# Kernel optimization log

Hardware: AMD Instinct MI355X
Metric: run time of the kernel (lower is better)

Reference implementation:

```python
import jax, jax.numpy as jnp
import numpy as np

NUM_EMBEDDINGS = 8192
EMBEDDING_DIM = 256
COMMITMENT_WEIGHT = 0.25
EMA_DECAY = 0.99
EPSILON = 1e-05


def setup_inputs() -> dict:
    key = jax.random.key(0)
    k1, k2 = jax.random.split(key)
    z = jax.random.normal(k1, (8, 4096, EMBEDDING_DIM), dtype=jnp.float32)
    # xavier-uniform-ish codebook init
    limit = np.sqrt(6.0 / (NUM_EMBEDDINGS + EMBEDDING_DIM))
    embeddings = jax.random.uniform(
        k2, (NUM_EMBEDDINGS, EMBEDDING_DIM), dtype=jnp.float32,
        minval=-limit, maxval=limit)
    ema_cluster_size = jnp.zeros((NUM_EMBEDDINGS,), dtype=jnp.float32)
    ema_embed_sum = embeddings.copy()
    return {
        'z': z,
        'embeddings': embeddings,
        'ema_cluster_size': ema_cluster_size,
        'ema_embed_sum': ema_embed_sum,
    }


def reference(z, embeddings, ema_cluster_size, ema_embed_sum):
    input_shape = z.shape
    D = input_shape[-1]
    z_flat = z.reshape(-1, D)                                  # [N, D]

    # Squared euclidean distances via expansion: ||z||^2 + ||e||^2 - 2 z.e
    z_sq = jnp.sum(z_flat * z_flat, axis=1, keepdims=True)     # [N, 1]
    e_sq = jnp.sum(embeddings * embeddings, axis=1)            # [K]
    ze = jnp.matmul(z_flat, embeddings.T)                      # [N, K]
    distances = z_sq + e_sq - 2.0 * ze                          # [N, K]
    indices = jnp.argmin(distances, axis=1)                    # [N] int

    z_q_flat = embeddings[indices]                             # [N, D] gather
    z_q = z_q_flat.reshape(input_shape)

    # commitment loss = mse(stop_grad(z_q), z)
    diff = jax.lax.stop_gradient(z_q) - z
    commitment_loss = jnp.mean(diff * diff) * COMMITMENT_WEIGHT

    # straight-through estimator
    z_q_st = z + jax.lax.stop_gradient(z_q - z)

    # EMA codebook update (functional version of the in-place buffer update)
    ones = jnp.ones_like(indices, dtype=embeddings.dtype)
    cluster_size = jax.ops.segment_sum(ones, indices, num_segments=NUM_EMBEDDINGS)
    embed_sum = jax.ops.segment_sum(z_flat, indices, num_segments=NUM_EMBEDDINGS)
    new_ema_cluster_size = EMA_DECAY * ema_cluster_size + (1.0 - EMA_DECAY) * cluster_size
    new_ema_embed_sum = EMA_DECAY * ema_embed_sum + (1.0 - EMA_DECAY) * embed_sum
    new_embeddings = new_ema_embed_sum / (new_ema_cluster_size[:, None] + EPSILON)

    indices_out = indices.reshape(input_shape[:-1])
    return (z_q_st, indices_out, commitment_loss,
            new_embeddings, new_ema_cluster_size, new_ema_embed_sum)
```

## Files before the change

### kernel.cpp

```cpp
#include <hip/hip_runtime.h>
#include <hip/hip_bf16.h>
#include <math.h>

#define N_TOK   32768
#define DIM     256
#define KC      8192

#define OUT_ZQ    0
#define OUT_IDX   8388608
#define OUT_LOSS  8421376
#define OUT_NEMB  8421377
#define OUT_CS    10518529
#define OUT_SUM   10526721

#define MARGIN  8e-3f
#define FLAGCAP 16384

typedef __attribute__((ext_vector_type(8))) __bf16 bf16x8;
typedef __attribute__((ext_vector_type(4))) float f32x4;

__device__ __forceinline__ void gload16(const void* g, void* l) {
  __builtin_amdgcn_global_load_lds((const __attribute__((address_space(1))) void*)g,
                                   (__attribute__((address_space(3))) void*)l, 16, 0, 0);
}

__device__ __forceinline__ float np_sumsq256(const float* __restrict__ p, int lane) {
  const int l = lane & 15;
  const int h = l >> 3;
  const int j = l & 7;
  const float* a = p + h * 128 + j;
  float x = a[0];
  float r = __fmul_rn(x, x);
  #pragma unroll
  for (int i = 1; i < 16; ++i) {
    x = a[8 * i];
    r = __fadd_rn(r, __fmul_rn(x, x));
  }
  r = __fadd_rn(r, __shfl_down(r, 1));
  r = __fadd_rn(r, __shfl_down(r, 2));
  r = __fadd_rn(r, __shfl_down(r, 4));
  float hi = __shfl(r, (lane & 48) | 8);
  return __fadd_rn(r, hi);
}

__global__ void vq_prep(const float* __restrict__ emb, float* __restrict__ esq,
                        short* __restrict__ esp2) {
  const int t = threadIdx.x;
  const int code = blockIdx.x * 8 + (t >> 5);
  const int p = t & 31, j = p >> 2, g = p & 3;
  const float* src = emb + (size_t)code * DIM + j * 32 + g * 8;
  const float4 v0 = *(const float4*)src;
  const float4 v1 = *(const float4*)(src + 4);
  const float xf[8] = {v0.x, v0.y, v0.z, v0.w, v1.x, v1.y, v1.z, v1.w};
  bf16x8 hb;
  #pragma unroll
  for (int e = 0; e < 8; ++e) hb[e] = (__bf16)xf[e];
  const int c = code & 15, sub = (code >> 4) & 3, ct = code >> 6;
  const int slot = (g + (c >> 1)) & 3;
  char* dst = (char*)esp2 + (size_t)ct * 32768 + ((sub * 8 + j) << 10) + c * 64 + slot * 16;
  *(bf16x8*)dst = hb;
  if (t < 128) {
    const int code2 = blockIdx.x * 8 + (t >> 4);
    const float s = np_sumsq256(emb + (size_t)code2 * DIM, t & 63);
    if ((t & 15) == 0) esq[code2] = s;
  }
}

__global__ void vq_transpose(const float* __restrict__ emb, float* __restrict__ embT) {
  __shared__ float t[64][65];
  const int tid = threadIdx.x;
  const int bc  = blockIdx.x & 127;
  const int bk  = blockIdx.x >> 7;
  const int cc0 = bc << 6, kc0 = bk << 6;
  const int col = tid & 63, qr = tid >> 6;
  #pragma unroll
  for (int i = 0; i < 16; ++i) {
    const int row = i * 4 + qr;
    t[row][col] = emb[(size_t)(cc0 + row) * DIM + kc0 + col];
  }
  __syncthreads();
  #pragma unroll
  for (int i = 0; i < 16; ++i) {
    const int krow = i * 4 + qr;
    embT[(size_t)(kc0 + krow) * KC + cc0 + col] = t[col][krow];
  }
}

__global__ void vq_init(int* __restrict__ hist, int* __restrict__ cnt) {
  const int i = blockIdx.x * blockDim.x + threadIdx.x;
  hist[i] = 0;
  if (i == 0) cnt[0] = 0;
}

__launch_bounds__(256, 4)
__global__ void vq_mfma(const float* __restrict__ z,
                        const short* __restrict__ esp,
                        const float* __restrict__ esq,
                        float* __restrict__ pb1,
                        int* __restrict__ pi1,
                        float* __restrict__ pb2) {
  __shared__ __align__(16) char lds[32768];
  const int tid  = threadIdx.x;
  const int lane = tid & 63;
  const int w    = tid >> 6;
  const int l15  = lane & 15;
  const int g    = lane >> 4;
  const int rt   = blockIdx.x >> 1;
  const int kh   = blockIdx.x & 1;
  const int rowbase = rt * 128 + w * 32;
  const int u0 = kh * 128, u1 = u0 + 128;
  const int gx = (g + (l15 >> 1)) & 3;
  const char* espb = (const char*)esp;

#define STAGE(U, BUFB)                                                           \
  {                                                                              \
    _Pragma("unroll")                                                            \
    for (int q_ = 0; q_ < 4; ++q_) {                                             \
      const int so_ = (((w << 2) + q_) << 10);                                   \
      gload16(espb + (size_t)(U) * 16384 + so_ + (lane << 4),                    \
              (void*)(lds + (BUFB) + so_));                                      \
    }                                                                            \
  }

  STAGE(u0, 0);

  bf16x8 Ahi[2][8];
  #pragma unroll
  for (int s = 0; s < 2; ++s) {
    const float* zr = z + (size_t)(rowbase + s * 16 + l15) * DIM + g * 8;
    #pragma unroll
    for (int c = 0; c < 8; ++c) {
      const float4 v0 = *(const float4*)(zr + c * 32);
      const float4 v1 = *(const float4*)(zr + c * 32 + 4);
      const float xf[8] = {v0.x, v0.y, v0.z, v0.w, v1.x, v1.y, v1.z, v1.w};
      #pragma unroll
      for (int e = 0; e < 8; ++e) Ahi[s][c][e] = (__bf16)xf[e];
    }
  }

  __syncthreads();

  float b1[2][4], b2[2][4];
  int   i1[2][4];
  #pragma unroll
  for (int s = 0; s < 2; ++s)
    #pragma unroll
    for (int r = 0; r < 4; ++r) { b1[s][r] = 3.4e38f; b2[s][r] = 3.4e38f; i1[s][r] = 0x7fffffff; }

  int bp = 0;
  for (int u = u0; u < u1; ++u) {
    if (u + 1 < u1) STAGE(u + 1, (bp ^ 1) << 14);

    const float eq0 = esq[(u << 5) + l15];
    const float eq1 = esq[(u << 5) + 16 + l15];

    f32x4 acc00 = (f32x4){0.f, 0.f, 0.f, 0.f};
    f32x4 acc01 = (f32x4){0.f, 0.f, 0.f, 0.f};
    f32x4 acc10 = (f32x4){0.f, 0.f, 0.f, 0.f};
    f32x4 acc11 = (f32x4){0.f, 0.f, 0.f, 0.f};

    {
      const char* base = lds + (bp << 14);
      #pragma unroll
      for (int j_ = 0; j_ < 8; ++j_) {
        const char* bq_ = base + (j_ << 10) + (l15 << 6) + (gx << 4);
        const bf16x8 bF0 = *(const bf16x8*)(bq_);
        const bf16x8 bF1 = *(const bf16x8*)(bq_ + 8192);
        acc00 = __builtin_amdgcn_mfma_f32_16x16x32_bf16(Ahi[0][j_], bF0, acc00, 0, 0, 0);
        acc01 = __builtin_amdgcn_mfma_f32_16x16x32_bf16(Ahi[0][j_], bF1, acc01, 0, 0, 0);
        acc10 = __builtin_amdgcn_mfma_f32_16x16x32_bf16(Ahi[1][j_], bF0, acc10, 0, 0, 0);
        acc11 = __builtin_amdgcn_mfma_f32_16x16x32_bf16(Ahi[1][j_], bF1, acc11, 0, 0, 0);
      }
    }

    const int code0 = (u << 5) + l15;
    const int code1 = code0 + 16;
    #pragma unroll
    for (int r = 0; r < 4; ++r) {
      const float sc = fmaf(-2.f, acc00[r], eq0);
      const bool lt = sc < b1[0][r];
      b2[0][r] = fminf(b2[0][r], fmaxf(sc, b1[0][r]));
      i1[0][r] = lt ? code0 : i1[0][r];
      b1[0][r] = fminf(b1[0][r], sc);
    }
    #pragma unroll
    for (int r = 0; r < 4; ++r) {
      const float sc = fmaf(-2.f, acc01[r], eq1);
      const bool lt = sc < b1[0][r];
      b2[0][r] = fminf(b2[0][r], fmaxf(sc, b1[0][r]));
      i1[0][r] = lt ? code1 : i1[0][r];
      b1[0][r] = fminf(b1[0][r], sc);
    }
    #pragma unroll
    for (int r = 0; r < 4; ++r) {
      const float sc = fmaf(-2.f, acc10[r], eq0);
      const bool lt = sc < b1[1][r];
      b2[1][r] = fminf(b2[1][r], fmaxf(sc, b1[1][r]));
      i1[1][r] = lt ? code0 : i1[1][r];
      b1[1][r] = fminf(b1[1][r], sc);
    }
    #pragma unroll
    for (int r = 0; r < 4; ++r) {
      const float sc = fmaf(-2.f, acc11[r], eq1);
      const bool lt = sc < b1[1][r];
      b2[1][r] = fminf(b2[1][r], fmaxf(sc, b1[1][r]));
      i1[1][r] = lt ? code1 : i1[1][r];
      b1[1][r] = fminf(b1[1][r], sc);
    }
    __syncthreads();
    bp ^= 1;
  }

  #pragma unroll
  for (int s = 0; s < 2; ++s) {
    #pragma unroll
    for (int r = 0; r < 4; ++r) {
      float v1 = b1[s][r], v2 = b2[s][r];
      int   j1 = i1[s][r];
      #pragma unroll
      for (int off = 1; off < 16; off <<= 1) {
        const float o1 = __shfl_xor(v1, off);
        const int   oj = __shfl_xor(j1, off);
        const float o2 = __shfl_xor(v2, off);
        v2 = fminf(fminf(v2, o2), fmaxf(v1, o1));
        const bool tk = (o1 < v1) || (o1 == v1 && oj < j1);
        j1 = tk ? oj : j1;
        v1 = fminf(v1, o1);
      }
      if (l15 == 0) {
        const int rr = kh * N_TOK + rowbase + s * 16 + (g << 2) + r;
        pb1[rr] = v1; pi1[rr] = j1; pb2[rr] = v2;
      }
    }
  }
}

__global__ void vq_merge(const float* __restrict__ pb1, const int* __restrict__ pi1,
                         const float* __restrict__ pb2, int* __restrict__ idxf,
                         int* __restrict__ flag, int* __restrict__ cnt) {
  const int gi = blockIdx.x * blockDim.x + threadIdx.x;
  const float va = pb1[gi],        vb = pb1[N_TOK + gi];
  const int   ia = pi1[gi],        ib = pi1[N_TOK + gi];
  const float v2a = pb2[gi],       v2b = pb2[N_TOK + gi];
  float v1, v2; int i1;
  if (va < vb || (va == vb && ia < ib)) { v1 = va; i1 = ia; v2 = fminf(v2a, vb); }
  else                                  { v1 = vb; i1 = ib; v2 = fminf(v2b, va); }
  idxf[gi] = i1;
  if (v2 - v1 < MARGIN) {
    const int p = atomicAdd(cnt, 1);
    if (p < FLAGCAP) flag[p] = gi;
  }
}

__global__ void vq_rescan2(const float* __restrict__ z,
                           const float* __restrict__ embT,
                           const float* __restrict__ esq,
                           const int* __restrict__ flag,
                           const int* __restrict__ cnt,
                           float* __restrict__ rpv,
                           int* __restrict__ rpi) {
  __shared__ __align__(16) float zT[DIM][16];
  __shared__ float zsq_sh[16];
  __shared__ float rv[4][16];
  __shared__ int   ri[4][16];
  __shared__ int   rown[16];
  int n = *cnt; if (n > FLAGCAP) n = FLAGCAP;
  const int tid = threadIdx.x;
  const int lane = tid & 63, wv = tid >> 6;
  const int nb = (n + 15) >> 4;
  const int ntask = nb * 8;
  for (int task = blockIdx.x; task < ntask; task += gridDim.x) {
    const int bb = task >> 3, cz = task & 7;
    __syncthreads();
    if (tid < 16) rown[tid] = flag[min(bb * 16 + tid, n - 1)];
    __syncthreads();
    #pragma unroll
    for (int rr = 0; rr < 16; ++rr) zT[tid][rr] = z[(size_t)rown[rr] * DIM + tid];
    {
      const int rr = tid >> 4;
      const float s = np_sumsq256(z + (size_t)rown[rr] * DIM, lane);
      if ((tid & 15) == 0) zsq_sh[rr] = s;
    }
    __syncthreads();

    float a[16][4];
    #pragma unroll
    for (int rr = 0; rr < 16; ++rr)
      #pragma unroll
      for (int q = 0; q < 4; ++q) a[rr][q] = 0.f;

    const int c0 = cz * 1024 + tid;
    #pragma unroll 2
    for (int k = 0; k < DIM; ++k) {
      const float* rk = embT + (size_t)k * KC + c0;
      const float e0 = rk[0], e1 = rk[256], e2 = rk[512], e3 = rk[768];
      const f32x4 z0 = *(const f32x4*)&zT[k][0];
      const f32x4 z1 = *(const f32x4*)&zT[k][4];
      const f32x4 z2 = *(const f32x4*)&zT[k][8];
      const f32x4 z3 = *(const f32x4*)&zT[k][12];
      #pragma unroll
      for (int r4 = 0; r4 < 4; ++r4) {
        a[r4][0] = fmaf(z0[r4], e0, a[r4][0]);
        a[r4][1] = fmaf(z0[r4], e1, a[r4][1]);
        a[r4][2] = fmaf(z0[r4], e2, a[r4][2]);
        a[r4][3] = fmaf(z0[r4], e3, a[r4][3]);
        a[4 + r4][0] = fmaf(z1[r4], e0, a[4 + r4][0]);
        a[4 + r4][1] = fmaf(z1[r4], e1, a[4 + r4][1]);
        a[4 + r4][2] = fmaf(z1[r4], e2, a[4 + r4][2]);
        a[4 + r4][3] = fmaf(z1[r4], e3, a[4 + r4][3]);
        a[8 + r4][0] = fmaf(z2[r4], e0, a[8 + r4][0]);
        a[8 + r4][1] = fmaf(z2[r4], e1, a[8 + r4][1]);
        a[8 + r4][2] = fmaf(z2[r4], e2, a[8 + r4][2]);
        a[8 + r4][3] = fmaf(z2[r4], e3, a[8 + r4][3]);
        a[12 + r4][0] = fmaf(z3[r4], e0, a[12 + r4][0]);
        a[12 + r4][1] = fmaf(z3[r4], e1, a[12 + r4][1]);
        a[12 + r4][2] = fmaf(z3[r4], e2, a[12 + r4][2]);
        a[12 + r4][3] = fmaf(z3[r4], e3, a[12 + r4][3]);
      }
    }

    #pragma unroll
    for (int rr = 0; rr < 16; ++rr) {
      float bv = 3.4e38f; int bi = 0x7fffffff;
      #pragma unroll
      for (int q = 0; q < 4; ++q) {
        const int code = cz * 1024 + q * 256 + tid;
        const float D = __fsub_rn(__fadd_rn(zsq_sh[rr], esq[code]), __fmul_rn(2.f, a[rr][q]));
        if (D < bv) { bv = D; bi = code; }
      }
      #pragma unroll
      for (int off = 32; off; off >>= 1) {
        const float ov = __shfl_down(bv, off);
        const int   oi = __shfl_down(bi, off);
        if (ov < bv || (ov == bv && oi < bi)) { bv = ov; bi = oi; }
      }
      if (lane == 0) { rv[wv][rr] = bv; ri[wv][rr] = bi; }
    }
    __syncthreads();
    if (tid < 16) {
      const int fi = bb * 16 + tid;
      if (fi < n) {
        float fv = rv[0][tid]; int fx = ri[0][tid];
        #pragma unroll
        for (int q = 1; q < 4; ++q)
          if (rv[q][tid] < fv || (rv[q][tid] == fv && ri[q][tid] < fx)) { fv = rv[q][tid]; fx = ri[q][tid]; }
        rpv[fi * 8 + cz] = fv; rpi[fi * 8 + cz] = fx;
      }
    }
  }
}

__global__ void vq_rmerge(const int* __restrict__ flag, const int* __restrict__ cnt,
                          const float* __restrict__ rpv, const int* __restrict__ rpi,
                          int* __restrict__ idxf) {
  int n = *cnt; if (n > FLAGCAP) n = FLAGCAP;
  const int fi = blockIdx.x * blockDim.x + threadIdx.x;
  if (fi >= n) return;
  float bv = rpv[fi * 8]; int bi = rpi[fi * 8];
  #pragma unroll
  for (int c = 1; c < 8; ++c) {
    const float v = rpv[fi * 8 + c]; const int ix = rpi[fi * 8 + c];
    if (v < bv || (v == bv && ix < bi)) { bv = v; bi = ix; }
  }
  idxf[flag[fi]] = bi;
}

__global__ void vq_gather(const float* __restrict__ z, const float* __restrict__ emb,
                          const int* __restrict__ idxf, float* __restrict__ out,
                          float* __restrict__ lossp, int* __restrict__ hist) {
  __shared__ float part[4];
  const int tid = threadIdx.x, lane = tid & 63, w = tid >> 6;
  const int row = blockIdx.x * 4 + w;
  const int code = idxf[row];
  const float4 zv = *(const float4*)(z + (size_t)row * DIM + lane * 4);
  const float4 ev = *(const float4*)(emb + (size_t)code * DIM + lane * 4);
  float4 d, o;
  d.x = ev.x - zv.x; d.y = ev.y - zv.y; d.z = ev.z - zv.z; d.w = ev.w - zv.w;
  o.x = zv.x + d.x;  o.y = zv.y + d.y;  o.z = zv.z + d.z;  o.w = zv.w + d.w;
  *(float4*)(out + OUT_ZQ + (size_t)row * DIM + lane * 4) = o;
  float sq = fmaf(d.x, d.x, fmaf(d.y, d.y, fmaf(d.z, d.z, d.w * d.w)));
  #pragma unroll
  for (int off = 32; off; off >>= 1) sq += __shfl_down(sq, off);
  if (lane == 0) {
    part[w] = sq;
    atomicAdd(hist + code, 1);
    out[OUT_IDX + row] = (float)code;
  }
  __syncthreads();
  if (tid == 0) lossp[blockIdx.x] = (part[0] + part[1]) + (part[2] + part[3]);
}

__global__ void vq_prefix(const float* __restrict__ ema_cs, int* __restrict__ hist,
                          int* __restrict__ base, int* __restrict__ cursor,
                          const float* __restrict__ lossp, float* __restrict__ out) {
  __shared__ int ps[256];
  __shared__ float lp[4];
  const int t = threadIdx.x;

  float ls = 0.f;
  #pragma unroll
  for (int j = 0; j < 8; ++j) {
    const float4 v = *(const float4*)(lossp + t * 32 + j * 4);
    ls += (v.x + v.y) + (v.z + v.w);
  }
  #pragma unroll
  for (int off = 32; off; off >>= 1) ls += __shfl_down(ls, off);
  if ((t & 63) == 0) lp[t >> 6] = ls;

  int loc[32]; int s = 0;
  #pragma unroll
  for (int j = 0; j < 32; ++j) { loc[j] = hist[t * 32 + j]; s += loc[j]; }
  ps[t] = s;
  __syncthreads();
  if (t == 0)
    out[OUT_LOSS] = 0.25f * (((lp[0] + lp[1]) + (lp[2] + lp[3])) * (1.f / 8388608.f));
  for (int off = 1; off < 256; off <<= 1) {
    const int v = (t >= off) ? ps[t - off] : 0;
    __syncthreads();
    ps[t] += v;
    __syncthreads();
  }
  int run = ps[t] - s;
  #pragma unroll
  for (int j = 0; j < 32; ++j) {
    const int i = t * 32 + j;
    base[i] = run; cursor[i] = run;
    out[OUT_CS + i] = 0.99f * ema_cs[i] + 0.01f * (float)loc[j];
    run += loc[j];
  }
}

__global__ void vq_slot(const int* __restrict__ idxf, int* __restrict__ cursor,
                        int* __restrict__ rowlist) {
  const int gi = blockIdx.x * blockDim.x + threadIdx.x;
  const int code = idxf[gi];
  const int p = atomicAdd(cursor + code, 1);
  rowlist[p] = gi;
}

__global__ void vq_embsum(const float* __restrict__ z, const float* __restrict__ ema_sum,
                          const int* __restrict__ rowlist, const int* __restrict__ base,
                          const int* __restrict__ hist, float* __restrict__ out) {
  const int code = blockIdx.x;
  const int lane = threadIdx.x;
  const int b = base[code], n = hist[code];
  float a0 = 0.f, a1 = 0.f, a2 = 0.f, a3 = 0.f;
  for (int i = 0; i < n; ++i) {
    const float4 v = *(const float4*)(z + (size_t)rowlist[b + i] * DIM + lane * 4);
    a0 += v.x; a1 += v.y; a2 += v.z; a3 += v.w;
  }
  const float4 es = *(const float4*)(ema_sum + (size_t)code * DIM + lane * 4);
  const float s0 = 0.99f * es.x + 0.01f * a0;
  const float s1 = 0.99f * es.y + 0.01f * a1;
  const float s2 = 0.99f * es.z + 0.01f * a2;
  const float s3 = 0.99f * es.w + 0.01f * a3;
  float* sp = out + OUT_SUM + (size_t)code * DIM + lane * 4;
  sp[0] = s0; sp[1] = s1; sp[2] = s2; sp[3] = s3;
  const float cs = out[OUT_CS + code] + 1e-5f;
  float* np_ = out + OUT_NEMB + (size_t)code * DIM + lane * 4;
  np_[0] = s0 / cs; np_[1] = s1 / cs; np_[2] = s2 / cs; np_[3] = s3 / cs;
}

extern "C" void kernel_launch(void* const* d_in, const int* in_sizes, int n_in,
                              void* d_out, int out_size, void* d_ws, size_t ws_size,
                              hipStream_t stream) {
  const float* z      = (const float*)d_in[0];
  const float* emb    = (const float*)d_in[1];
  const float* emacs  = (const float*)d_in[2];
  const float* emasum = (const float*)d_in[3];
  float* out = (float*)d_out;
  float* ws  = (float*)d_ws;

  float* esq     = ws;
  int*   idxf    = (int*)(ws + 8192);
  int*   flag    = (int*)(ws + 40960);
  int*   cnt     = (int*)(ws + 57344);
  int*   hist    = (int*)(ws + 57600);
  int*   base    = (int*)(ws + 65792);
  int*   cursor  = (int*)(ws + 73984);
  int*   rowlist = (int*)(ws + 82176);
  float* pb1     = ws + 114944;
  int*   pi1     = (int*)(ws + 180480);
  float* pb2     = ws + 246016;
  short* esp2    = (short*)(ws + 311552);
  float* embT    = ws + 1360128;
  float* rpv     = ws + 3457280;
  int*   rpi     = (int*)(ws + 3588352);
  float* lossp   = pb1;

  vq_prep<<<KC / 8, 256, 0, stream>>>(emb, esq, esp2);
  vq_transpose<<<512, 256, 0, stream>>>(emb, embT);
  vq_init<<<KC / 256, 256, 0, stream>>>(hist, cnt);

  vq_mfma<<<512, 256, 0, stream>>>(z, esp2, esq, pb1, pi1, pb2);
  vq_merge<<<N_TOK / 256, 256, 0, stream>>>(pb1, pi1, pb2, idxf, flag, cnt);
  vq_rescan2<<<1024, 256, 0, stream>>>(z, embT, esq, flag, cnt, rpv, rpi);
  vq_rmerge<<<FLAGCAP / 256, 256, 0, stream>>>(flag, cnt, rpv, rpi, idxf);

  vq_gather<<<N_TOK / 4, 256, 0, stream>>>(z, emb, idxf, out, lossp, hist);
  vq_prefix<<<1, 256, 0, stream>>>(emacs, hist, base, cursor, lossp, out);
  vq_slot<<<N_TOK / 256, 256, 0, stream>>>(idxf, cursor, rowlist);
  vq_embsum<<<KC, 64, 0, stream>>>(z, emasum, rowlist, base, hist, out);
}
```

Baseline: 341.8 us.

## Split codebook search four ways across blocks and fold init into prep

The distance/argmin kernel now splits the codebook into four quarters per row tile instead of two, doubling the grid to 1024 blocks for better CU occupancy on the large GPU. The merge kernel combines four partial top-2 results, and workspace offsets are enlarged for the bigger partial buffers. Separately, the histogram/counter init kernel is removed and its zeroing folded into the prep kernel to save a launch. The trade-off is more partial-result traffic and redundant A-tile loads (z reloaded per quarter).

```diff
diff --git a/kernel.cpp b/kernel.cpp
--- a/kernel.cpp
+++ b/kernel.cpp
@@ -44,7 +44,8 @@
 }
 
 __global__ void vq_prep(const float* __restrict__ emb, float* __restrict__ esq,
-                        short* __restrict__ esp2) {
+                        short* __restrict__ esp2, int* __restrict__ hist,
+                        int* __restrict__ cnt) {
   const int t = threadIdx.x;
   const int code = blockIdx.x * 8 + (t >> 5);
   const int p = t & 31, j = p >> 2, g = p & 3;
@@ -64,6 +65,8 @@
     const float s = np_sumsq256(emb + (size_t)code2 * DIM, t & 63);
     if ((t & 15) == 0) esq[code2] = s;
   }
+  if (blockIdx.x < 32) hist[blockIdx.x * 256 + t] = 0;
+  if (blockIdx.x == 0 && t == 0) cnt[0] = 0;
 }
 
 __global__ void vq_transpose(const float* __restrict__ emb, float* __restrict__ embT) {
@@ -84,12 +87,6 @@
     const int krow = i * 4 + qr;
     embT[(size_t)(kc0 + krow) * KC + cc0 + col] = t[col][krow];
   }
-}
-
-__global__ void vq_init(int* __restrict__ hist, int* __restrict__ cnt) {
-  const int i = blockIdx.x * blockDim.x + threadIdx.x;
-  hist[i] = 0;
-  if (i == 0) cnt[0] = 0;
 }
 
 __launch_bounds__(256, 4)
@@ -105,10 +102,10 @@
   const int w    = tid >> 6;
   const int l15  = lane & 15;
   const int g    = lane >> 4;
-  const int rt   = blockIdx.x >> 1;
-  const int kh   = blockIdx.x & 1;
+  const int rt   = blockIdx.x >> 2;
+  const int kh   = blockIdx.x & 3;
   const int rowbase = rt * 128 + w * 32;
-  const int u0 = kh * 128, u1 = u0 + 128;
+  const int u0 = kh * 64, u1 = u0 + 64;
   const int gx = (g + (l15 >> 1)) & 3;
   const char* espb = (const char*)esp;
 
@@ -239,12 +236,20 @@
                          const float* __restrict__ pb2, int* __restrict__ idxf,
                          int* __restrict__ flag, int* __restrict__ cnt) {
   const int gi = blockIdx.x * blockDim.x + threadIdx.x;
-  const float va = pb1[gi],        vb = pb1[N_TOK + gi];
-  const int   ia = pi1[gi],        ib = pi1[N_TOK + gi];
-  const float v2a = pb2[gi],       v2b = pb2[N_TOK + gi];
-  float v1, v2; int i1;
-  if (va < vb || (va == vb && ia < ib)) { v1 = va; i1 = ia; v2 = fminf(v2a, vb); }
-  else                                  { v1 = vb; i1 = ib; v2 = fminf(v2b, va); }
+  float v1 = pb1[gi], v2 = pb2[gi];
+  int   i1 = pi1[gi];
+  #pragma unroll
+  for (int h = 1; h < 4; ++h) {
+    const float o1 = pb1[h * N_TOK + gi];
+    const int   oj = pi1[h * N_TOK + gi];
+    const float o2 = pb2[h * N_TOK + gi];
+    if (o1 < v1 || (o1 == v1 && oj < i1)) {
+      v2 = fminf(v1, o2);
+      v1 = o1; i1 = oj;
+    } else {
+      v2 = fminf(v2, o1);
+    }
+  }
   idxf[gi] = i1;
   if (v2 - v1 < MARGIN) {
     const int p = atomicAdd(cnt, 1);
@@ -480,19 +485,18 @@
   int*   cursor  = (int*)(ws + 73984);
   int*   rowlist = (int*)(ws + 82176);
   float* pb1     = ws + 114944;
-  int*   pi1     = (int*)(ws + 180480);
-  float* pb2     = ws + 246016;
-  short* esp2    = (short*)(ws + 311552);
-  float* embT    = ws + 1360128;
-  float* rpv     = ws + 3457280;
-  int*   rpi     = (int*)(ws + 3588352);
+  int*   pi1     = (int*)(ws + 246016);
+  float* pb2     = ws + 377088;
+  short* esp2    = (short*)(ws + 508160);
+  float* embT    = ws + 1556736;
+  float* rpv     = ws + 3653888;
+  int*   rpi     = (int*)(ws + 3784960);
   float* lossp   = pb1;
 
-  vq_prep<<<KC / 8, 256, 0, stream>>>(emb, esq, esp2);
+  vq_prep<<<KC / 8, 256, 0, stream>>>(emb, esq, esp2, hist, cnt);
   vq_transpose<<<512, 256, 0, stream>>>(emb, embT);
-  vq_init<<<KC / 256, 256, 0, stream>>>(hist, cnt);
-
-  vq_mfma<<<512, 256, 0, stream>>>(z, esp2, esq, pb1, pi1, pb2);
+
+  vq_mfma<<<1024, 256, 0, stream>>>(z, esp2, esq, pb1, pi1, pb2);
   vq_merge<<<N_TOK / 256, 256, 0, stream>>>(pb1, pi1, pb2, idxf, flag, cnt);
   vq_rescan2<<<1024, 256, 0, stream>>>(z, embT, esq, flag, cnt, rpv, rpi);
   vq_rmerge<<<FLAGCAP / 256, 256, 0, stream>>>(flag, cnt, rpv, rpi, idxf);
```

New measurement: 331.6 us. 1.03x faster.
